# Optimization experiments

Measured on AMD Instinct MI355X. Metric: run time of the kernel, lower is better.

## Reference

```python
import jax, jax.numpy as jnp
import numpy as np

B, T, C, H = 2, 2048, 1024, 16
HD = C // H  # head dim = 64


def setup_inputs() -> dict:
    key = jax.random.key(0)
    k1, k2, k3 = jax.random.split(key, 3)
    scale = 0.02
    x = jax.random.normal(k1, (B, T, C), dtype=jnp.float32)
    w_attn = jax.random.normal(k2, (C, 3 * C), dtype=jnp.float32) * scale
    b_attn = jnp.zeros((3 * C,), dtype=jnp.float32)
    w_proj = jax.random.normal(k3, (C, C), dtype=jnp.float32) * scale
    b_proj = jnp.zeros((C,), dtype=jnp.float32)
    return {"x": x, "w_attn": w_attn, "b_attn": b_attn, "w_proj": w_proj, "b_proj": b_proj}


def reference(x, w_attn, b_attn, w_proj, b_proj):
    b, t, c = x.shape
    qkv = x @ w_attn + b_attn  # [B,T,3C]
    q, k, v = jnp.split(qkv, 3, axis=-1)
    # [B,T,C] -> [B,H,T,HD]
    q = q.reshape(b, t, H, HD).transpose(0, 2, 1, 3)
    k = k.reshape(b, t, H, HD).transpose(0, 2, 1, 3)
    v = v.reshape(b, t, H, HD).transpose(0, 2, 1, 3)
    att = jnp.einsum('bhqd,bhkd->bhqk', q, k) * (1.0 / jnp.sqrt(jnp.float32(HD)))
    causal = jnp.tril(jnp.ones((t, t), dtype=bool))  # [T,T]
    att = jnp.where(causal[None, None, :, :], att, jnp.float32(-jnp.inf))
    att = jax.nn.softmax(att, axis=-1)
    y = jnp.einsum('bhqk,bhkd->bhqd', att, v)
    y = y.transpose(0, 2, 1, 3).reshape(b, t, c)
    return y @ w_proj + b_proj
```

## Files before the change

### kernel.cpp

```cpp
#include <hip/hip_runtime.h>


typedef unsigned short u16;
typedef unsigned short u16x8 __attribute__((ext_vector_type(8)));
typedef __bf16 bf16x8 __attribute__((ext_vector_type(8)));
typedef float f32x4 __attribute__((ext_vector_type(4)));

#define MFMA16(a, b, c) __builtin_amdgcn_mfma_f32_16x16x32_bf16(a, b, c, 0, 0, 0)

static __device__ __forceinline__ u16 f2b(float f) {
  union { float f; unsigned int i; } x; x.f = f;
  unsigned int r = x.i + 0x7fffu + ((x.i >> 16) & 1u);
  return (u16)(r >> 16);
}
static __device__ __forceinline__ u16 f2b_trunc(float f) {
  union { float f; unsigned int i; } x; x.f = f;
  return (u16)(x.i >> 16);
}

__global__ __launch_bounds__(256) void cast_f32_bf16(
    const float* __restrict__ in, u16* __restrict__ out) {
  int i = (blockIdx.x * 256 + threadIdx.x) * 8;
  float4 a = *(const float4*)&in[i];
  float4 b = *(const float4*)&in[i + 4];
  u16x8 o;
  o[0] = f2b(a.x); o[1] = f2b(a.y); o[2] = f2b(a.z); o[3] = f2b(a.w);
  o[4] = f2b(b.x); o[5] = f2b(b.y); o[6] = f2b(b.z); o[7] = f2b(b.w);
  *(u16x8*)&out[i] = o;
}

__global__ __launch_bounds__(256) void transpose_f32_bf16(
    const float* __restrict__ in, u16* __restrict__ out, int R, int Cc) {
  __shared__ u16 tile[32][33];
  int bx = blockIdx.x, by = blockIdx.y;
  int tx = threadIdx.x, ty = threadIdx.y;
#pragma unroll
  for (int i = 0; i < 4; i++) {
    int r = by * 32 + ty + i * 8;
    int c = bx * 32 + tx;
    tile[ty + i * 8][tx] = f2b(in[r * Cc + c]);
  }
  __syncthreads();
#pragma unroll
  for (int i = 0; i < 4; i++) {
    int r = bx * 32 + ty + i * 8;
    int c = by * 32 + tx;
    out[r * R + c] = tile[tx][ty + i * 8];
  }
}

__global__ __launch_bounds__(256) void transpose_v(
    const u16* __restrict__ in, u16* __restrict__ out) {
  int bh = blockIdx.y;
  int t = blockIdx.x * 128 + (threadIdx.x & 127);
  int dg = (threadIdx.x >> 7) * 32;
  const u16* src = in + (bh * 2048 + t) * 64;
  u16* dst = out + bh * 64 * 2048 + t;
#pragma unroll
  for (int i = 0; i < 32; i++) {
    int d = dg + i;
    dst[d * 2048] = src[d];
  }
}

template <int MODE>
__global__ __launch_bounds__(256, 2) void gemm_bt(
    const u16* __restrict__ A, const u16* __restrict__ Bt,
    const float* __restrict__ bias, float* __restrict__ out,
    u16* __restrict__ Qb, u16* __restrict__ Kb, u16* __restrict__ Vb,
    int M, int N, int K) {
  __shared__ u16 lA[128 * 40];
  __shared__ u16 lB[128 * 40];

  const int tid = threadIdx.x;
  const int lane = tid & 63;
  const int w = tid >> 6;
  const int wm = (w >> 1) * 64, wn = (w & 1) * 64;
  const int l15 = lane & 15, quad = lane >> 4;
  const int m0 = blockIdx.y * 128, n0 = blockIdx.x * 128;

  const int srow = tid >> 2;
  const int scol = (tid & 3) * 8;

  f32x4 acc[4][4] = {};

  for (int k0 = 0; k0 < K; k0 += 32) {
    __syncthreads();
#pragma unroll
    for (int h = 0; h < 2; h++) {
      int r = srow + h * 64;
      *(u16x8*)&lA[r * 40 + scol] = *(const u16x8*)&A[(m0 + r) * K + k0 + scol];
      *(u16x8*)&lB[r * 40 + scol] = *(const u16x8*)&Bt[(n0 + r) * K + k0 + scol];
    }
    __syncthreads();

    bf16x8 af[4], bfr[4];
#pragma unroll
    for (int mi = 0; mi < 4; mi++)
      af[mi] = *(const bf16x8*)&lA[(wm + mi * 16 + l15) * 40 + quad * 8];
#pragma unroll
    for (int ni = 0; ni < 4; ni++)
      bfr[ni] = *(const bf16x8*)&lB[(wn + ni * 16 + l15) * 40 + quad * 8];
#pragma unroll
    for (int mi = 0; mi < 4; mi++)
#pragma unroll
      for (int ni = 0; ni < 4; ni++)
        acc[mi][ni] = MFMA16(af[mi], bfr[ni], acc[mi][ni]);
  }

#pragma unroll
  for (int mi = 0; mi < 4; mi++) {
#pragma unroll
    for (int ni = 0; ni < 4; ni++) {
      int n = n0 + wn + ni * 16 + l15;
      float bv = bias[n];
#pragma unroll
      for (int reg = 0; reg < 4; reg++) {
        int m = m0 + wm + mi * 16 + quad * 4 + reg;
        float v = acc[mi][ni][reg] + bv;
        if (MODE == 1) {
          out[m * N + n] = v;
        } else {
          int which = n >> 10;
          if (which == 1) v *= 0.18033688011112042f;
          int hn = n & 1023;
          int hh = hn >> 6, d = hn & 63;
          int b = m >> 11, t = m & 2047;
          u16* dst = (which == 0) ? Qb : ((which == 1) ? Kb : Vb);
          dst[(((b << 4) + hh) * 2048 + t) * 64 + d] = f2b(v);
        }
      }
    }
  }
}

__global__ __launch_bounds__(256, 4) void attn_kernel(
    const u16* __restrict__ Qg, const u16* __restrict__ Kg,
    const u16* __restrict__ Vt, u16* __restrict__ Yg) {
  __shared__ u16 lk[64 * 72];
  __shared__ u16 lvt[64 * 72];
  __shared__ u16 lp[4][16 * 72];

  const int qt = 31 - blockIdx.x;
  const int bh = blockIdx.y;
  const int tid = threadIdx.x;
  const int lane = tid & 63;
  const int w = tid >> 6;
  const int l15 = lane & 15, quad = lane >> 4;
  const int qbase = qt * 64;
  const int base = bh * 2048 * 64;
  const int vbase = bh * 64 * 2048;

  const int sr = tid >> 3;
  const int sc = (tid & 7) * 8;

  const u16* qrow = Qg + base + (qbase + w * 16 + l15) * 64;
  bf16x8 aq0 = *(const bf16x8*)&qrow[quad * 8];
  bf16x8 aq1 = *(const bf16x8*)&qrow[32 + quad * 8];

  u16x8 onesu = {0x3F80, 0x3F80, 0x3F80, 0x3F80, 0x3F80, 0x3F80, 0x3F80, 0x3F80};
  bf16x8 ones = *(const bf16x8*)&onesu;

  const u16* kp = Kg + base;
  const u16* vp = Vt + vbase;

  u16x8 kr[2], vr[2];
#pragma unroll
  for (int h = 0; h < 2; h++) {
    int r = sr + h * 32;
    kr[h] = *(const u16x8*)&kp[r * 64 + sc];
    vr[h] = *(const u16x8*)&vp[r * 2048 + sc];
  }

  u16* lpw = &lp[w][0];
  f32x4 oacc[4] = {};
  f32x4 lacc = {};

  for (int kt = 0; kt <= qt; kt++) {
    __syncthreads();
#pragma unroll
    for (int h = 0; h < 2; h++) {
      int r = sr + h * 32;
      *(u16x8*)&lk[r * 72 + sc] = kr[h];
      *(u16x8*)&lvt[r * 72 + sc] = vr[h];
    }
    __syncthreads();
    if (kt < qt) {
      int kvb = (kt + 1) * 64;
#pragma unroll
      for (int h = 0; h < 2; h++) {
        int r = sr + h * 32;
        kr[h] = *(const u16x8*)&kp[(kvb + r) * 64 + sc];
        vr[h] = *(const u16x8*)&vp[r * 2048 + kvb + sc];
      }
    }

    f32x4 sa[4] = {};
#pragma unroll
    for (int nt = 0; nt < 4; nt++) {
      bf16x8 bk0 = *(const bf16x8*)&lk[(nt * 16 + l15) * 72 + quad * 8];
      bf16x8 bk1 = *(const bf16x8*)&lk[(nt * 16 + l15) * 72 + 32 + quad * 8];
      sa[nt] = MFMA16(aq0, bk0, sa[nt]);
      sa[nt] = MFMA16(aq1, bk1, sa[nt]);
    }

    const bool diag = (kt == qt);
#pragma unroll
    for (int nt = 0; nt < 4; nt++) {
      int kcol = nt * 16 + l15;
#pragma unroll
      for (int reg = 0; reg < 4; reg++) {
        float s = sa[nt][reg];
        if (diag) {
          int qr = w * 16 + quad * 4 + reg;
          if (kcol > qr) s = -1e30f;
        }
        lpw[(quad * 4 + reg) * 72 + nt * 16 + l15] = f2b_trunc(exp2f(s));
      }
    }

    bf16x8 pa0 = *(const bf16x8*)&lpw[l15 * 72 + quad * 8];
    bf16x8 pa1 = *(const bf16x8*)&lpw[l15 * 72 + 32 + quad * 8];

    lacc = MFMA16(pa0, ones, lacc);
    lacc = MFMA16(pa1, ones, lacc);
#pragma unroll
    for (int dt = 0; dt < 4; dt++) {
      bf16x8 bv0 = *(const bf16x8*)&lvt[(dt * 16 + l15) * 72 + quad * 8];
      bf16x8 bv1 = *(const bf16x8*)&lvt[(dt * 16 + l15) * 72 + 32 + quad * 8];
      oacc[dt] = MFMA16(pa0, bv0, oacc[dt]);
      oacc[dt] = MFMA16(pa1, bv1, oacc[dt]);
    }
  }

  const int b = bh >> 4, hh = bh & 15;
  float inv[4];
#pragma unroll
  for (int reg = 0; reg < 4; reg++) inv[reg] = 1.0f / lacc[reg];
#pragma unroll
  for (int dt = 0; dt < 4; dt++)
#pragma unroll
    for (int reg = 0; reg < 4; reg++) {
      int q = qbase + w * 16 + quad * 4 + reg;
      int col = hh * 64 + dt * 16 + l15;
      Yg[(b * 2048 + q) * 1024 + col] = f2b(oacc[dt][reg] * inv[reg]);
    }
}

extern "C" void kernel_launch(void* const* d_in, const int* in_sizes, int n_in,
                              void* d_out, int out_size, void* d_ws, size_t ws_size,
                              hipStream_t stream) {
  const float* x      = (const float*)d_in[0];
  const float* w_attn = (const float*)d_in[1];
  const float* b_attn = (const float*)d_in[2];
  const float* w_proj = (const float*)d_in[3];
  const float* b_proj = (const float*)d_in[4];
  float* out = (float*)d_out;

  char* ws = (char*)d_ws;
  u16* wattnT = (u16*)(ws);
  u16* wprojT = (u16*)(ws + 6291456);
  u16* xb     = (u16*)(ws + 8388608);
  u16* Vt     = xb;
  u16* Qb     = (u16*)(ws + 16777216);
  u16* Kb     = (u16*)(ws + 25165824);
  u16* Vb     = (u16*)(ws + 33554432);
  u16* Yb     = (u16*)(ws + 41943040);

  cast_f32_bf16<<<2048, 256, 0, stream>>>(x, xb);
  transpose_f32_bf16<<<dim3(96, 32), dim3(32, 8), 0, stream>>>(w_attn, wattnT, 1024, 3072);
  transpose_f32_bf16<<<dim3(32, 32), dim3(32, 8), 0, stream>>>(w_proj, wprojT, 1024, 1024);
  gemm_bt<0><<<dim3(24, 32), 256, 0, stream>>>(xb, wattnT, b_attn, nullptr,
                                               Qb, Kb, Vb, 4096, 3072, 1024);
  transpose_v<<<dim3(16, 32), 256, 0, stream>>>(Vb, Vt);
  attn_kernel<<<dim3(32, 32), 256, 0, stream>>>(Qb, Kb, Vt, Yb);
  gemm_bt<1><<<dim3(8, 32), 256, 0, stream>>>(Yb, wprojT, b_proj, out,
                                              nullptr, nullptr, nullptr, 4096, 1024, 1024);
}
```

Measured before the change: 224.8 us.

## Keep attention probabilities in registers and load GEMM tiles directly to LDS

The attention kernel now computes S transposed (K as the A operand, Q as the B operand), so each lane's exp2 outputs already sit in the layout the PV MFMA expects. This removes the per-wave LDS round trip for P and the extra MFMAs that summed rows against a ones vector; the row sum is instead accumulated in scalars and reduced with shuffles. The V fragments are repacked from two 4-element loads to match the permuted k ordering. Separately, the GEMM stages tiles through global_load_lds without padding. That drops the register hop on the way into LDS but may add LDS bank conflicts on the unpadded fragment reads.

After: 217.2 us. 1.03x faster.

```diff
diff --git a/kernel.cpp b/kernel.cpp
--- a/kernel.cpp
+++ b/kernel.cpp
@@ -4,6 +4,7 @@
 typedef unsigned short u16;
 typedef unsigned short u16x8 __attribute__((ext_vector_type(8)));
 typedef __bf16 bf16x8 __attribute__((ext_vector_type(8)));
+typedef __bf16 bf16x4 __attribute__((ext_vector_type(4)));
 typedef float f32x4 __attribute__((ext_vector_type(4)));
 
 #define MFMA16(a, b, c) __builtin_amdgcn_mfma_f32_16x16x32_bf16(a, b, c, 0, 0, 0)
@@ -13,9 +14,16 @@
   unsigned int r = x.i + 0x7fffu + ((x.i >> 16) & 1u);
   return (u16)(r >> 16);
 }
-static __device__ __forceinline__ u16 f2b_trunc(float f) {
-  union { float f; unsigned int i; } x; x.f = f;
-  return (u16)(x.i >> 16);
+
+static __device__ __forceinline__ void gload_lds16(const u16* g, u16* l) {
+#if defined(__HIP_DEVICE_COMPILE__)
+  __builtin_amdgcn_global_load_lds(
+      (const __attribute__((address_space(1))) unsigned int*)g,
+      (__attribute__((address_space(3))) unsigned int*)l,
+      16, 0, 0);
+#else
+  (void)g; (void)l;
+#endif
 }
 
 __global__ __launch_bounds__(256) void cast_f32_bf16(
@@ -69,8 +77,8 @@
     const float* __restrict__ bias, float* __restrict__ out,
     u16* __restrict__ Qb, u16* __restrict__ Kb, u16* __restrict__ Vb,
     int M, int N, int K) {
-  __shared__ u16 lA[128 * 40];
-  __shared__ u16 lB[128 * 40];
+  __shared__ u16 lA[128 * 32];
+  __shared__ u16 lB[128 * 32];
 
   const int tid = threadIdx.x;
   const int lane = tid & 63;
@@ -79,8 +87,8 @@
   const int l15 = lane & 15, quad = lane >> 4;
   const int m0 = blockIdx.y * 128, n0 = blockIdx.x * 128;
 
-  const int srow = tid >> 2;
-  const int scol = (tid & 3) * 8;
+  const int srow = lane >> 2;
+  const int scol = (lane & 3) * 8;
 
   f32x4 acc[4][4] = {};
 
@@ -88,19 +96,19 @@
     __syncthreads();
 #pragma unroll
     for (int h = 0; h < 2; h++) {
-      int r = srow + h * 64;
-      *(u16x8*)&lA[r * 40 + scol] = *(const u16x8*)&A[(m0 + r) * K + k0 + scol];
-      *(u16x8*)&lB[r * 40 + scol] = *(const u16x8*)&Bt[(n0 + r) * K + k0 + scol];
+      int r = h * 64 + w * 16 + srow;
+      gload_lds16(&A[(m0 + r) * K + k0 + scol], &lA[h * 2048 + w * 512 + lane * 8]);
+      gload_lds16(&Bt[(n0 + r) * K + k0 + scol], &lB[h * 2048 + w * 512 + lane * 8]);
     }
     __syncthreads();
 
     bf16x8 af[4], bfr[4];
 #pragma unroll
     for (int mi = 0; mi < 4; mi++)
-      af[mi] = *(const bf16x8*)&lA[(wm + mi * 16 + l15) * 40 + quad * 8];
+      af[mi] = *(const bf16x8*)&lA[(wm + mi * 16 + l15) * 32 + quad * 8];
 #pragma unroll
     for (int ni = 0; ni < 4; ni++)
-      bfr[ni] = *(const bf16x8*)&lB[(wn + ni * 16 + l15) * 40 + quad * 8];
+      bfr[ni] = *(const bf16x8*)&lB[(wn + ni * 16 + l15) * 32 + quad * 8];
 #pragma unroll
     for (int mi = 0; mi < 4; mi++)
 #pragma unroll
@@ -139,7 +147,6 @@
     const u16* __restrict__ Vt, u16* __restrict__ Yg) {
   __shared__ u16 lk[64 * 72];
   __shared__ u16 lvt[64 * 72];
-  __shared__ u16 lp[4][16 * 72];
 
   const int qt = 31 - blockIdx.x;
   const int bh = blockIdx.y;
@@ -155,11 +162,8 @@
   const int sc = (tid & 7) * 8;
 
   const u16* qrow = Qg + base + (qbase + w * 16 + l15) * 64;
-  bf16x8 aq0 = *(const bf16x8*)&qrow[quad * 8];
-  bf16x8 aq1 = *(const bf16x8*)&qrow[32 + quad * 8];
-
-  u16x8 onesu = {0x3F80, 0x3F80, 0x3F80, 0x3F80, 0x3F80, 0x3F80, 0x3F80, 0x3F80};
-  bf16x8 ones = *(const bf16x8*)&onesu;
+  bf16x8 bq0 = *(const bf16x8*)&qrow[quad * 8];
+  bf16x8 bq1 = *(const bf16x8*)&qrow[32 + quad * 8];
 
   const u16* kp = Kg + base;
   const u16* vp = Vt + vbase;
@@ -172,9 +176,8 @@
     vr[h] = *(const u16x8*)&vp[r * 2048 + sc];
   }
 
-  u16* lpw = &lp[w][0];
   f32x4 oacc[4] = {};
-  f32x4 lacc = {};
+  float ls = 0.f;
 
   for (int kt = 0; kt <= qt; kt++) {
     __syncthreads();
@@ -195,48 +198,53 @@
       }
     }
 
-    f32x4 sa[4] = {};
-#pragma unroll
-    for (int nt = 0; nt < 4; nt++) {
-      bf16x8 bk0 = *(const bf16x8*)&lk[(nt * 16 + l15) * 72 + quad * 8];
-      bf16x8 bk1 = *(const bf16x8*)&lk[(nt * 16 + l15) * 72 + 32 + quad * 8];
-      sa[nt] = MFMA16(aq0, bk0, sa[nt]);
-      sa[nt] = MFMA16(aq1, bk1, sa[nt]);
-    }
-
     const bool diag = (kt == qt);
-#pragma unroll
-    for (int nt = 0; nt < 4; nt++) {
-      int kcol = nt * 16 + l15;
-#pragma unroll
-      for (int reg = 0; reg < 4; reg++) {
-        float s = sa[nt][reg];
-        if (diag) {
-          int qr = w * 16 + quad * 4 + reg;
-          if (kcol > qr) s = -1e30f;
+    const int qloc = w * 16 + l15;
+
+#pragma unroll
+    for (int u = 0; u < 2; u++) {
+      bf16x8 pa;
+      float psum = 0.f;
+#pragma unroll
+      for (int half = 0; half < 2; half++) {
+        int nt = 2 * u + half;
+        bf16x8 ak0 = *(const bf16x8*)&lk[(nt * 16 + l15) * 72 + quad * 8];
+        bf16x8 ak1 = *(const bf16x8*)&lk[(nt * 16 + l15) * 72 + 32 + quad * 8];
+        f32x4 st = {};
+        st = MFMA16(ak0, bq0, st);
+        st = MFMA16(ak1, bq1, st);
+#pragma unroll
+        for (int reg = 0; reg < 4; reg++) {
+          float s = st[reg];
+          if (diag && (nt * 16 + quad * 4 + reg) > qloc) s = -1e30f;
+          float p = exp2f(s);
+          psum += p;
+          pa[half * 4 + reg] = (__bf16)p;
         }
-        lpw[(quad * 4 + reg) * 72 + nt * 16 + l15] = f2b_trunc(exp2f(s));
-      }
-    }
-
-    bf16x8 pa0 = *(const bf16x8*)&lpw[l15 * 72 + quad * 8];
-    bf16x8 pa1 = *(const bf16x8*)&lpw[l15 * 72 + 32 + quad * 8];
-
-    lacc = MFMA16(pa0, ones, lacc);
-    lacc = MFMA16(pa1, ones, lacc);
-#pragma unroll
-    for (int dt = 0; dt < 4; dt++) {
-      bf16x8 bv0 = *(const bf16x8*)&lvt[(dt * 16 + l15) * 72 + quad * 8];
-      bf16x8 bv1 = *(const bf16x8*)&lvt[(dt * 16 + l15) * 72 + 32 + quad * 8];
-      oacc[dt] = MFMA16(pa0, bv0, oacc[dt]);
-      oacc[dt] = MFMA16(pa1, bv1, oacc[dt]);
-    }
-  }
+      }
+      ls += psum;
+
+#pragma unroll
+      for (int dt = 0; dt < 4; dt++) {
+        const u16* vrow = &lvt[(dt * 16 + l15) * 72 + u * 32 + quad * 4];
+        bf16x4 lo = *(const bf16x4*)&vrow[0];
+        bf16x4 hi = *(const bf16x4*)&vrow[16];
+        bf16x8 bv;
+#pragma unroll
+        for (int j = 0; j < 4; j++) { bv[j] = lo[j]; bv[4 + j] = hi[j]; }
+        oacc[dt] = MFMA16(pa, bv, oacc[dt]);
+      }
+    }
+  }
+
+  ls += __shfl_xor(ls, 16, 64);
+  ls += __shfl_xor(ls, 32, 64);
 
   const int b = bh >> 4, hh = bh & 15;
   float inv[4];
 #pragma unroll
-  for (int reg = 0; reg < 4; reg++) inv[reg] = 1.0f / lacc[reg];
+  for (int reg = 0; reg < 4; reg++)
+    inv[reg] = 1.0f / __shfl(ls, quad * 4 + reg, 64);
 #pragma unroll
   for (int dt = 0; dt < 4; dt++)
 #pragma unroll
```
